# Kernel tuning notes

Hardware: AMD Instinct MI355X
Metric: run time of the kernel (lower is better)

## Reference

```python
import jax, jax.numpy as jnp
import numpy as np

N = 8192
D = 256
E = 131072


def setup_inputs() -> dict:
    key = jax.random.key(0)
    k1, k2 = jax.random.split(key)
    l_enc = jax.random.normal(k1, (N, D), dtype=jnp.float32)
    edge_index = jax.random.randint(k2, (2, E), 0, N, dtype=jnp.int64)
    return {"l_enc": l_enc, "edge_index": edge_index}


def reference(l_enc, edge_index):
    n = l_enc.shape[0]
    dt = l_enc.dtype
    # Vectorized symmetric adjacency build (replaces the per-edge Python loop).
    adj = (
        jnp.zeros((n, n), dtype=dt)
        .at[edge_index[0], edge_index[1]].set(1.0)
        .at[edge_index[1], edge_index[0]].set(1.0)
    )
    # Dense Gram matrix + sigmoid, diagonal zeroed like (1 - eye) * res.
    res = jax.nn.sigmoid(jnp.matmul(l_enc, l_enc.T))
    mask = jnp.eye(n, dtype=dt)
    res = (1.0 - mask) * res
    # BCE with torch-style log clamp at -100 (handles res == 0 on the diagonal).
    log_p = jnp.maximum(jnp.log(res), -100.0)
    log_1mp = jnp.maximum(jnp.log1p(-res), -100.0)
    return jnp.mean(-(adj * log_p + (1.0 - adj) * log_1mp))
```

## Files before the change

### kernel.cpp

```cpp
#include <hip/hip_runtime.h>
#include <hip/hip_bf16.h>

#define NN 8192
#define DK 256
#define NE 131072
#define T128 64
#define NBLK (T128*(T128+1)/2)

typedef __attribute__((ext_vector_type(8))) short bf16x8;
typedef __attribute__((ext_vector_type(4))) float f32x4;
typedef const __attribute__((address_space(1))) void* gas1_t;
typedef __attribute__((address_space(3))) void* las3_t;

__device__ __align__(16) unsigned       g_mask[(size_t)NN*NN/32];
__device__ __align__(16) unsigned short g_bf[(size_t)NN*DK];
__device__ __align__(16) double g_part[NBLK];

__device__ __forceinline__ unsigned short f2bf(float f) {
    unsigned u = __float_as_uint(f);
    unsigned r = (u + 0x7FFFu + ((u >> 16) & 1u)) >> 16;
    return (unsigned short)r;
}

__global__ void k_convscat(const float* __restrict__ x,
                           const long long* __restrict__ ei) {
    int i = blockIdx.x * 256 + threadIdx.x;
    float4 v = ((const float4*)x)[i];
    ushort4 b;
    b.x = f2bf(v.x); b.y = f2bf(v.y); b.z = f2bf(v.z); b.w = f2bf(v.w);
    *(ushort4*)(&g_bf[(size_t)i * 4]) = b;
    if (blockIdx.x < NE / 256) {
        int e = blockIdx.x * 256 + threadIdx.x;
        int ii = (int)ei[e];
        int jj = (int)ei[NE + e];
        atomicOr(&g_mask[(size_t)ii * (NN/32) + (jj >> 5)], 1u << (jj & 31));
        atomicOr(&g_mask[(size_t)jj * (NN/32) + (ii >> 5)], 1u << (ii & 31));
    }
}

__global__ __launch_bounds__(256, 3) void k_loss() {
    __shared__ __align__(16) unsigned short lsA[128 * 64];
    __shared__ __align__(16) unsigned short lsB[128 * 64];
    __shared__ double s_part[4];

    int orig = blockIdx.x;
    int bid  = (orig & 7) * (NBLK / 8) + (orig >> 3);
    int rem = bid, ti = 0;
    while (rem >= T128 - ti) { rem -= T128 - ti; ++ti; }
    int tj = ti + rem;

    const int tid  = threadIdx.x;
    const int lane = tid & 63;
    const int w    = tid >> 6;
    const int wr   = w >> 1;
    const int wc   = w & 1;
    const int lr   = lane & 15;
    const int lq   = lane >> 4;

    const int gq = (tid & 7) ^ ((tid >> 3) & 7);
    const unsigned short* srcA0 = g_bf + (size_t)(ti * 128 + (tid >> 3)) * DK + gq * 8;
    const size_t dB = (size_t)(tj - ti) * 128 * DK;
    const int lds0 = tid * 8;

#define STAGE(kt) do {                                                             \
    _Pragma("unroll")                                                              \
    for (int i = 0; i < 4; ++i) {                                                  \
        __builtin_amdgcn_global_load_lds(                                          \
            (gas1_t)(const void*)(srcA0 + (size_t)i * 32 * DK + (kt) * 64),        \
            (las3_t)(void*)&lsA[lds0 + i * 2048], 16, 0, 0);                       \
        __builtin_amdgcn_global_load_lds(                                          \
            (gas1_t)(const void*)(srcA0 + dB + (size_t)i * 32 * DK + (kt) * 64),   \
            (las3_t)(void*)&lsB[lds0 + i * 2048], 16, 0, 0);                       \
    }                                                                              \
} while (0)

    f32x4 acc[4][4] = {};

    STAGE(0);
    __syncthreads();

    #pragma unroll
    for (int kt = 0; kt < 4; ++kt) {
        #pragma unroll
        for (int ks = 0; ks < 2; ++ks) {
            const int cq = (ks * 4 + lq) ^ (lr & 7);
            bf16x8 fa[4];
            #pragma unroll
            for (int fm = 0; fm < 4; ++fm) {
                int ra = wr * 64 + fm * 16 + lr;
                fa[fm] = *(const bf16x8*)((const char*)&lsA[0] + ra * 128 + cq * 16);
            }
            #pragma unroll
            for (int fn = 0; fn < 4; ++fn) {
                int rb = wc * 64 + fn * 16 + lr;
                bf16x8 fbv = *(const bf16x8*)((const char*)&lsB[0] + rb * 128 + cq * 16);
                #pragma unroll
                for (int fm = 0; fm < 4; ++fm)
                    acc[fm][fn] = __builtin_amdgcn_mfma_f32_16x16x32_bf16(
                        fa[fm], fbv, acc[fm][fn], 0, 0, 0);
            }
        }
        if (kt < 3) {
            __syncthreads();
            STAGE(kt + 1);
            __syncthreads();
        }
    }
#undef STAGE

    const int R0 = ti * 128 + wr * 64;
    const int C0 = tj * 128 + wc * 64;
    const char* mrow0 = (const char*)g_mask + (size_t)(C0 >> 5) * 4;
    const bool diagB = (ti == tj) && (wr == wc);
    float tsum = 0.0f;
    #pragma unroll
    for (int fm = 0; fm < 4; ++fm) {
        #pragma unroll
        for (int r2 = 0; r2 < 4; ++r2) {
            int rowg = R0 + fm * 16 + lq * 4 + r2;
            uint2 m2 = *(const uint2*)(mrow0 + (size_t)rowg * (NN / 8));
            #pragma unroll
            for (int fn = 0; fn < 4; ++fn) {
                float s = acc[fm][fn][r2];
                unsigned mw = (fn & 2) ? m2.y : m2.x;
                bool bit = ((mw >> ((fn & 1) * 16 + lr)) & 1) != 0;
                float x  = bit ? -s : s;
                float wv = x * 1.44269504f;
                float e2 = __builtin_amdgcn_exp2f(fminf(wv, 126.0f));
                float t  = 0.6931471805599453f * __builtin_amdgcn_logf(1.0f + e2);
                float thr = bit ? 128.0f : 24.0f;
                float term = (wv >= thr) ? 100.0f : t;
                if (diagB && fm == fn && (lq * 4 + r2) == lr)
                    term = bit ? 100.0f : 0.0f;
                tsum += term;
            }
        }
    }
    #pragma unroll
    for (int off = 32; off; off >>= 1) tsum += __shfl_down(tsum, off);
    if (lane == 0) {
        float wgt = (ti == tj) ? 1.0f : 2.0f;
        s_part[w] = (double)(tsum * wgt);
    }
    __syncthreads();
    if (tid == 0)
        g_part[orig] = (s_part[0] + s_part[1]) + (s_part[2] + s_part[3]);
}

__global__ void k_final(float* __restrict__ out) {
    __shared__ double sd[256];
    double s = 0.0;
    for (int i = threadIdx.x; i < NBLK; i += 256) s += g_part[i];
    sd[threadIdx.x] = s;
    __syncthreads();
    #pragma unroll
    for (int st = 128; st; st >>= 1) {
        if (threadIdx.x < st) sd[threadIdx.x] += sd[threadIdx.x + st];
        __syncthreads();
    }
    if (threadIdx.x == 0)
        out[0] = (float)(sd[0] * (1.0 / ((double)NN * (double)NN)));
}

extern "C" void kernel_launch(void* const* d_in, const int* in_sizes, int n_in,
                              void* d_out, int out_size, void* d_ws, size_t ws_size,
                              hipStream_t stream) {
    const float* l_enc = (const float*)d_in[0];
    const long long* ei = (const long long*)d_in[1];
    float* out = (float*)d_out;

    void* mask_ptr = nullptr;
    hipGetSymbolAddress(&mask_ptr, HIP_SYMBOL(g_mask));
    hipMemsetAsync(mask_ptr, 0, (size_t)NN * NN / 8, stream);

    k_convscat<<<2048, 256, 0, stream>>>(l_enc, ei);
    k_loss<<<NBLK, 256, 0, stream>>>();
    k_final<<<1, 256, 0, stream>>>(out);
}
```

Measured before the change: 61.96 us.

## Move adjacency handling to a sparse edge-correction pass and drop the mask memset

The dense loss kernel now computes only the no-edge softplus term for every pair and no longer reads the bitmask. A new sparse kernel walks the edges, clears each set bit atomically so duplicates count once, and adds the positive-edge minus negative-edge difference using a scalar bf16 dot product. It also removes the diagonal contributions. Because the correction pass leaves the mask zeroed, the 8 MB memset per call is dropped, which relies on the mask starting at zero on first use. The change removes the mask reads and branches from the hot epilogue, at the cost of an extra kernel and per-edge dot products.

```diff
diff --git a/kernel.cpp b/kernel.cpp
--- a/kernel.cpp
+++ b/kernel.cpp
@@ -6,6 +6,10 @@
 #define NE 131072
 #define T128 64
 #define NBLK (T128*(T128+1)/2)
+#define NCORR 544
+#define L2E 1.44269504f
+#define SAT_L2 144.269504f
+#define LN2D 0.6931471805599453
 
 typedef __attribute__((ext_vector_type(8))) short bf16x8;
 typedef __attribute__((ext_vector_type(4))) float f32x4;
@@ -14,12 +18,40 @@
 
 __device__ __align__(16) unsigned       g_mask[(size_t)NN*NN/32];
 __device__ __align__(16) unsigned short g_bf[(size_t)NN*DK];
-__device__ __align__(16) double g_part[NBLK];
+__device__ __align__(16) double g_part[NBLK + NCORR];
 
 __device__ __forceinline__ unsigned short f2bf(float f) {
     unsigned u = __float_as_uint(f);
     unsigned r = (u + 0x7FFFu + ((u >> 16) & 1u)) >> 16;
     return (unsigned short)r;
+}
+
+__device__ __forceinline__ float base_l2(float s) {
+    float wv = s * L2E;
+    float e2 = __builtin_amdgcn_exp2f(wv);
+    float l  = __builtin_amdgcn_logf(1.0f + e2);
+    return (wv >= 24.0f) ? SAT_L2 : l;
+}
+__device__ __forceinline__ float term1_l2(float s) {
+    float wv = s * L2E;
+    float e2 = __builtin_amdgcn_exp2f(fminf(wv, 126.0f));
+    float l  = __builtin_amdgcn_logf(1.0f + e2);
+    float t1 = fmaxf(l - wv, 0.0f);
+    return (wv <= -128.0f) ? SAT_L2 : t1;
+}
+__device__ __forceinline__ float dotrow(int a, int b) {
+    const uint2* ra = (const uint2*)(g_bf + (size_t)a * DK);
+    const uint2* rb = (const uint2*)(g_bf + (size_t)b * DK);
+    float s = 0.0f;
+    #pragma unroll 8
+    for (int k = 0; k < 64; ++k) {
+        uint2 va = ra[k], vb = rb[k];
+        s = fmaf(__uint_as_float(va.x << 16),          __uint_as_float(vb.x << 16),          s);
+        s = fmaf(__uint_as_float(va.x & 0xffff0000u),  __uint_as_float(vb.x & 0xffff0000u),  s);
+        s = fmaf(__uint_as_float(va.y << 16),          __uint_as_float(vb.y << 16),          s);
+        s = fmaf(__uint_as_float(va.y & 0xffff0000u),  __uint_as_float(vb.y & 0xffff0000u),  s);
+    }
+    return s;
 }
 
 __global__ void k_convscat(const float* __restrict__ x,
@@ -38,6 +70,44 @@
     }
 }
 
+__global__ void k_corr(const long long* __restrict__ ei) {
+    __shared__ double s_part[4];
+    const int tid = threadIdx.x, lane = tid & 63, w = tid >> 6;
+    float corr = 0.0f;
+    if (blockIdx.x < 512) {
+        int e = blockIdx.x * 256 + tid;
+        int a = (int)ei[e], b = (int)ei[NE + e];
+        unsigned m1 = 1u << (b & 31);
+        unsigned o1 = atomicAnd(&g_mask[(size_t)a * (NN/32) + (b >> 5)], ~m1);
+        bool c1 = (o1 & m1) != 0;
+        bool c2 = false;
+        if (a != b) {
+            unsigned m2 = 1u << (a & 31);
+            unsigned o2 = atomicAnd(&g_mask[(size_t)b * (NN/32) + (a >> 5)], ~m2);
+            c2 = (o2 & m2) != 0;
+        }
+        if (c1 | c2) {
+            if (a == b) {
+                corr = SAT_L2;
+            } else {
+                float s = dotrow(a, b);
+                float d = term1_l2(s) - base_l2(s);
+                corr = d * ((c1 ? 1.0f : 0.0f) + (c2 ? 1.0f : 0.0f));
+            }
+        }
+    } else {
+        int r = (blockIdx.x - 512) * 256 + tid;
+        corr = -base_l2(dotrow(r, r));
+    }
+    #pragma unroll
+    for (int off = 32; off; off >>= 1) corr += __shfl_down(corr, off);
+    if (lane == 0) s_part[w] = (double)corr;
+    __syncthreads();
+    if (tid == 0)
+        g_part[NBLK + blockIdx.x] =
+            ((s_part[0] + s_part[1]) + (s_part[2] + s_part[3])) * LN2D;
+}
+
 __global__ __launch_bounds__(256, 3) void k_loss() {
     __shared__ __align__(16) unsigned short lsA[128 * 64];
     __shared__ __align__(16) unsigned short lsB[128 * 64];
@@ -108,49 +178,35 @@
     }
 #undef STAGE
 
-    const int R0 = ti * 128 + wr * 64;
-    const int C0 = tj * 128 + wc * 64;
-    const char* mrow0 = (const char*)g_mask + (size_t)(C0 >> 5) * 4;
-    const bool diagB = (ti == tj) && (wr == wc);
     float tsum = 0.0f;
     #pragma unroll
     for (int fm = 0; fm < 4; ++fm) {
         #pragma unroll
         for (int r2 = 0; r2 < 4; ++r2) {
-            int rowg = R0 + fm * 16 + lq * 4 + r2;
-            uint2 m2 = *(const uint2*)(mrow0 + (size_t)rowg * (NN / 8));
             #pragma unroll
             for (int fn = 0; fn < 4; ++fn) {
-                float s = acc[fm][fn][r2];
-                unsigned mw = (fn & 2) ? m2.y : m2.x;
-                bool bit = ((mw >> ((fn & 1) * 16 + lr)) & 1) != 0;
-                float x  = bit ? -s : s;
-                float wv = x * 1.44269504f;
-                float e2 = __builtin_amdgcn_exp2f(fminf(wv, 126.0f));
-                float t  = 0.6931471805599453f * __builtin_amdgcn_logf(1.0f + e2);
-                float thr = bit ? 128.0f : 24.0f;
-                float term = (wv >= thr) ? 100.0f : t;
-                if (diagB && fm == fn && (lq * 4 + r2) == lr)
-                    term = bit ? 100.0f : 0.0f;
-                tsum += term;
+                float s  = acc[fm][fn][r2];
+                float wv = s * L2E;
+                float e2 = __builtin_amdgcn_exp2f(wv);
+                float l  = __builtin_amdgcn_logf(1.0f + e2);
+                tsum += (wv >= 24.0f) ? SAT_L2 : l;
             }
         }
     }
     #pragma unroll
     for (int off = 32; off; off >>= 1) tsum += __shfl_down(tsum, off);
-    if (lane == 0) {
-        float wgt = (ti == tj) ? 1.0f : 2.0f;
-        s_part[w] = (double)(tsum * wgt);
-    }
-    __syncthreads();
-    if (tid == 0)
-        g_part[orig] = (s_part[0] + s_part[1]) + (s_part[2] + s_part[3]);
+    if (lane == 0) s_part[w] = (double)tsum;
+    __syncthreads();
+    if (tid == 0) {
+        double wgt = (ti == tj) ? LN2D : 2.0 * LN2D;
+        g_part[orig] = ((s_part[0] + s_part[1]) + (s_part[2] + s_part[3])) * wgt;
+    }
 }
 
 __global__ void k_final(float* __restrict__ out) {
     __shared__ double sd[256];
     double s = 0.0;
-    for (int i = threadIdx.x; i < NBLK; i += 256) s += g_part[i];
+    for (int i = threadIdx.x; i < NBLK + NCORR; i += 256) s += g_part[i];
     sd[threadIdx.x] = s;
     __syncthreads();
     #pragma unroll
@@ -169,11 +225,8 @@
     const long long* ei = (const long long*)d_in[1];
     float* out = (float*)d_out;
 
-    void* mask_ptr = nullptr;
-    hipGetSymbolAddress(&mask_ptr, HIP_SYMBOL(g_mask));
-    hipMemsetAsync(mask_ptr, 0, (size_t)NN * NN / 8, stream);
-
     k_convscat<<<2048, 256, 0, stream>>>(l_enc, ei);
+    k_corr<<<NCORR, 256, 0, stream>>>(ei);
     k_loss<<<NBLK, 256, 0, stream>>>();
     k_final<<<1, 256, 0, stream>>>(out);
 }
```

New measurement: 60.88 us. Within noise of the previous version (-1.7%).

## Drop mask memset via self-clearing mask, prefetch mask bits, store upper-triangle edges

Applied to the files above, without the earlier changes.

The per-call 8 MB memset of the adjacency bitmask is removed. Instead, the loss kernel zeroes any nonzero mask words it has consumed, so the buffer returns to all-zero for the next call. Edges that cross 128-row tiles are now written only once, into the upper-triangle tile the loss kernel actually reads. Mask words are loaded before the GEMM so their latency overlaps the matrix math, and the ln2 scale and clamp are moved into the per-block reduction. In exchange, correctness now depends on the mask starting at zero and on every call running to completion.

```diff
diff --git a/kernel.cpp b/kernel.cpp
--- a/kernel.cpp
+++ b/kernel.cpp
@@ -6,6 +6,9 @@
 #define NE 131072
 #define T128 64
 #define NBLK (T128*(T128+1)/2)
+#define L2E 1.44269504f
+#define SAT_L2 144.269504f
+#define LN2D 0.6931471805599453
 
 typedef __attribute__((ext_vector_type(8))) short bf16x8;
 typedef __attribute__((ext_vector_type(4))) float f32x4;
@@ -31,10 +34,15 @@
     *(ushort4*)(&g_bf[(size_t)i * 4]) = b;
     if (blockIdx.x < NE / 256) {
         int e = blockIdx.x * 256 + threadIdx.x;
-        int ii = (int)ei[e];
-        int jj = (int)ei[NE + e];
-        atomicOr(&g_mask[(size_t)ii * (NN/32) + (jj >> 5)], 1u << (jj & 31));
-        atomicOr(&g_mask[(size_t)jj * (NN/32) + (ii >> 5)], 1u << (ii & 31));
+        int a = (int)ei[e];
+        int bb = (int)ei[NE + e];
+        if ((a >> 7) == (bb >> 7)) {
+            atomicOr(&g_mask[(size_t)a  * (NN/32) + (bb >> 5)], 1u << (bb & 31));
+            atomicOr(&g_mask[(size_t)bb * (NN/32) + (a  >> 5)], 1u << (a  & 31));
+        } else {
+            int lo = min(a, bb), hi = max(a, bb);
+            atomicOr(&g_mask[(size_t)lo * (NN/32) + (hi >> 5)], 1u << (hi & 31));
+        }
     }
 }
 
@@ -77,6 +85,16 @@
     f32x4 acc[4][4] = {};
 
     STAGE(0);
+    const int R0 = ti * 128 + wr * 64;
+    const int C0 = tj * 128 + wc * 64;
+    uint2 m2p[4][4];
+    #pragma unroll
+    for (int fm = 0; fm < 4; ++fm)
+        #pragma unroll
+        for (int r2 = 0; r2 < 4; ++r2) {
+            int rowg = R0 + fm * 16 + lq * 4 + r2;
+            m2p[fm][r2] = *(const uint2*)(g_mask + (size_t)rowg * (NN/32) + (C0 >> 5));
+        }
     __syncthreads();
 
     #pragma unroll
@@ -108,43 +126,51 @@
     }
 #undef STAGE
 
-    const int R0 = ti * 128 + wr * 64;
-    const int C0 = tj * 128 + wc * 64;
-    const char* mrow0 = (const char*)g_mask + (size_t)(C0 >> 5) * 4;
     const bool diagB = (ti == tj) && (wr == wc);
     float tsum = 0.0f;
     #pragma unroll
     for (int fm = 0; fm < 4; ++fm) {
         #pragma unroll
         for (int r2 = 0; r2 < 4; ++r2) {
-            int rowg = R0 + fm * 16 + lq * 4 + r2;
-            uint2 m2 = *(const uint2*)(mrow0 + (size_t)rowg * (NN / 8));
+            uint2 m2 = m2p[fm][r2];
             #pragma unroll
             for (int fn = 0; fn < 4; ++fn) {
                 float s = acc[fm][fn][r2];
                 unsigned mw = (fn & 2) ? m2.y : m2.x;
                 bool bit = ((mw >> ((fn & 1) * 16 + lr)) & 1) != 0;
-                float x  = bit ? -s : s;
-                float wv = x * 1.44269504f;
-                float e2 = __builtin_amdgcn_exp2f(fminf(wv, 126.0f));
-                float t  = 0.6931471805599453f * __builtin_amdgcn_logf(1.0f + e2);
+                float wv = s * L2E;
+                float aw = bit ? -wv : wv;
+                float e2 = __builtin_amdgcn_exp2f(aw);
+                float l  = __builtin_amdgcn_logf(1.0f + e2);
                 float thr = bit ? 128.0f : 24.0f;
-                float term = (wv >= thr) ? 100.0f : t;
+                float term = (aw >= thr) ? SAT_L2 : l;
                 if (diagB && fm == fn && (lq * 4 + r2) == lr)
-                    term = bit ? 100.0f : 0.0f;
+                    term = bit ? SAT_L2 : 0.0f;
                 tsum += term;
             }
         }
     }
+    if (lr == 0) {
+        #pragma unroll
+        for (int fm = 0; fm < 4; ++fm)
+            #pragma unroll
+            for (int r2 = 0; r2 < 4; ++r2) {
+                uint2 m2 = m2p[fm][r2];
+                if (m2.x | m2.y) {
+                    int rowg = R0 + fm * 16 + lq * 4 + r2;
+                    uint2 z; z.x = 0u; z.y = 0u;
+                    *(uint2*)(g_mask + (size_t)rowg * (NN/32) + (C0 >> 5)) = z;
+                }
+            }
+    }
     #pragma unroll
     for (int off = 32; off; off >>= 1) tsum += __shfl_down(tsum, off);
-    if (lane == 0) {
-        float wgt = (ti == tj) ? 1.0f : 2.0f;
-        s_part[w] = (double)(tsum * wgt);
-    }
+    if (lane == 0) s_part[w] = (double)tsum;
     __syncthreads();
-    if (tid == 0)
-        g_part[orig] = (s_part[0] + s_part[1]) + (s_part[2] + s_part[3]);
+    if (tid == 0) {
+        double wgt = (ti == tj) ? LN2D : 2.0 * LN2D;
+        g_part[orig] = ((s_part[0] + s_part[1]) + (s_part[2] + s_part[3])) * wgt;
+    }
 }
 
 __global__ void k_final(float* __restrict__ out) {
@@ -169,10 +195,6 @@
     const long long* ei = (const long long*)d_in[1];
     float* out = (float*)d_out;
 
-    void* mask_ptr = nullptr;
-    hipGetSymbolAddress(&mask_ptr, HIP_SYMBOL(g_mask));
-    hipMemsetAsync(mask_ptr, 0, (size_t)NN * NN / 8, stream);
-
     k_convscat<<<2048, 256, 0, stream>>>(l_enc, ei);
     k_loss<<<NBLK, 256, 0, stream>>>();
     k_final<<<1, 256, 0, stream>>>(out);
```

Result: faster. 59.80 us (-3.5%).
